# Performance work log

Measured on AMD Instinct MI355X. Metric: run time of the kernel, lower is better.

Reference implementation:

```python
import jax, jax.numpy as jnp
import numpy as np

N_EMBD = 512
NUM_HEADS = 8
HEAD_SIZE = 64


def setup_inputs() -> dict:
    key = jax.random.key(0)
    ks = jax.random.split(key, 6)
    B, T, C, H, D = 64, 256, N_EMBD, NUM_HEADS, HEAD_SIZE
    s = 0.02
    return {
        "x": jax.random.normal(ks[0], (B, T, C), dtype=jnp.float32),
        "wq": jax.random.normal(ks[1], (H, C, D), dtype=jnp.float32) * s,
        "wk": jax.random.normal(ks[2], (H, C, D), dtype=jnp.float32) * s,
        "wv": jax.random.normal(ks[3], (H, C, D), dtype=jnp.float32) * s,
        "bq": jnp.zeros((H, D), dtype=jnp.float32),
        "bk": jnp.zeros((H, D), dtype=jnp.float32),
        "bv": jnp.zeros((H, D), dtype=jnp.float32),
        "wo": jax.random.normal(ks[4], (H * D, C), dtype=jnp.float32) * s,
        "bo": jnp.zeros((C,), dtype=jnp.float32),
    }


def reference(x, wq, wk, wv, bq, bk, bv, wo, bo):
    B, T, C = x.shape
    H, _, D = wq.shape
    # per-head QKV projections (vectorized over heads)
    q = jnp.einsum('btc,hcd->bhtd', x, wq) + bq[None, :, None, :]
    k = jnp.einsum('btc,hcd->bhtd', x, wk) + bk[None, :, None, :]
    v = jnp.einsum('btc,hcd->bhtd', x, wv) + bv[None, :, None, :]
    scale = 1.0 / jnp.sqrt(jnp.asarray(D, dtype=x.dtype))
    scores = jnp.einsum('bhtd,bhsd->bhts', q, k) * scale  # [B,H,T,T]
    causal = jnp.tril(jnp.ones((T, T), dtype=bool))
    scores = jnp.where(causal[None, None], scores, -jnp.inf)
    weights = jax.nn.softmax(scores, axis=-1)  # dropout omitted (eval mode)
    out = jnp.einsum('bhts,bhsd->bhtd', weights, v)  # [B,H,T,D]
    combined = out.transpose(0, 2, 1, 3).reshape(B, T, H * D)
    return combined @ wo + bo
```

## Files before the change

### kernel.cpp

```cpp
#include <hip/hip_runtime.h>

typedef unsigned int   u32;
typedef unsigned short u16;
typedef __attribute__((ext_vector_type(8))) short short8;
typedef __attribute__((ext_vector_type(4))) float f32x4;


__device__ __forceinline__ u16 f2bf(float f) {
    u32 u = __float_as_uint(f);
    u += 0x7fffu + ((u >> 16) & 1u);
    return (u16)(u >> 16);
}

__device__ __forceinline__ void gload_lds16(const u16* g, u16* l) {
    __builtin_amdgcn_global_load_lds(
        (const __attribute__((address_space(1))) u32*)(const void*)g,
        (__attribute__((address_space(3))) u32*)(void*)l, 16, 0, 0);
}

__global__ void cast_x_kernel(const float* __restrict__ x, u16* __restrict__ xb) {
    int i = blockIdx.x * 256 + threadIdx.x;
    float4 v = ((const float4*)x)[i];
    ushort4 o;
    o.x = f2bf(v.x); o.y = f2bf(v.y); o.z = f2bf(v.z); o.w = f2bf(v.w);
    ((ushort4*)xb)[i] = o;
}

__global__ void pack_wqkv_kernel(const float* __restrict__ wq, const float* __restrict__ wk,
                                 const float* __restrict__ wv, u16* __restrict__ wt) {
    int i = blockIdx.x * 256 + threadIdx.x;
    int n = i >> 9, c = i & 511;
    int proj = n >> 9, hd = n & 511;
    int h = hd >> 6, d = hd & 63;
    const float* w = (proj == 0) ? wq : (proj == 1) ? wk : wv;
    wt[(size_t)n * 512 + c] = f2bf(w[h * 32768 + c * 64 + d]);
}

__global__ void pack_wo_kernel(const float* __restrict__ wo, u16* __restrict__ wt) {
    int i = blockIdx.x * 256 + threadIdx.x;
    int n = i >> 9, k = i & 511;
    wt[(size_t)n * 512 + k] = f2bf(wo[(size_t)k * 512 + n]);
}

template<int EPI, int NT>
__global__ __launch_bounds__(256)
void gemm128_kernel(const u16* __restrict__ A, const u16* __restrict__ Bt,
                    float* __restrict__ outf, const float* __restrict__ bo,
                    u16* __restrict__ Qb, u16* __restrict__ Kb, u16* __restrict__ Vb,
                    const float* __restrict__ bq, const float* __restrict__ bk,
                    const float* __restrict__ bv) {
    __shared__ __align__(16) u16 As[3][128 * 32];
    __shared__ __align__(16) u16 Bs[3][128 * 32];
    const int tid = threadIdx.x;
    const int bid = blockIdx.x;
    const int xcd = bid & 7;
    const int k8  = bid >> 3;
    const int m0 = (xcd * 16 + k8 / NT) * 128;
    const int n0 = (k8 % NT) * 128;
    const int lrow = tid >> 2;
    const int seg  = tid & 3;
    const int xsw  = (lrow >> 1) & 3;
    const u16* Ag = A  + (size_t)(m0 + lrow) * 512 + (seg ^ xsw) * 8;
    const u16* Bg = Bt + (size_t)(n0 + lrow) * 512 + (seg ^ xsw) * 8;
    const int lofs = lrow * 32 + seg * 8;

    const int w = tid >> 6, lane = tid & 63;
    const int wrow = (w >> 1) * 64, wcol = (w & 1) * 64;
    const int lm = lane & 15, quad = lane >> 4;
    const int kx = (quad ^ ((lm >> 1) & 3)) * 8;

    f32x4 acc[4][4] = {};

    gload_lds16(Ag,            As[0] + lofs);
    gload_lds16(Ag + 64 * 512, As[0] + lofs + 64 * 32);
    gload_lds16(Bg,            Bs[0] + lofs);
    gload_lds16(Bg + 64 * 512, Bs[0] + lofs + 64 * 32);

    #pragma unroll 1
    for (int kt = 0; kt < 16; ++kt) {
        __syncthreads();
        if (kt < 15) {
            const u16* Agp = Ag + (kt + 1) * 32;
            const u16* Bgp = Bg + (kt + 1) * 32;
            u16* Asp = As[(kt + 1) % 3] + lofs;
            u16* Bsp = Bs[(kt + 1) % 3] + lofs;
            gload_lds16(Agp,            Asp);
            gload_lds16(Agp + 64 * 512, Asp + 64 * 32);
            gload_lds16(Bgp,            Bsp);
            gload_lds16(Bgp + 64 * 512, Bsp + 64 * 32);
        }
        const u16* Ac = As[kt % 3];
        const u16* Bc = Bs[kt % 3];
        short8 af[4], bf[4];
        #pragma unroll
        for (int mi = 0; mi < 4; ++mi)
            af[mi] = *(const short8*)(Ac + (wrow + mi * 16 + lm) * 32 + kx);
        #pragma unroll
        for (int ni = 0; ni < 4; ++ni)
            bf[ni] = *(const short8*)(Bc + (wcol + ni * 16 + lm) * 32 + kx);
        #pragma unroll
        for (int mi = 0; mi < 4; ++mi)
            #pragma unroll
            for (int ni = 0; ni < 4; ++ni)
                acc[mi][ni] = __builtin_amdgcn_mfma_f32_16x16x32_bf16(af[mi], bf[ni], acc[mi][ni], 0, 0, 0);
    }

    if (EPI == 1) {
        #pragma unroll
        for (int ni = 0; ni < 4; ++ni) {
            int ncol = n0 + wcol + ni * 16 + lm;
            float bias = bo[ncol];
            #pragma unroll
            for (int mi = 0; mi < 4; ++mi) {
                int mbase = m0 + wrow + mi * 16 + quad * 4;
                #pragma unroll
                for (int r = 0; r < 4; ++r)
                    outf[(size_t)(mbase + r) * 512 + ncol] = acc[mi][ni][r] + bias;
            }
        }
    } else {
        #pragma unroll
        for (int ni = 0; ni < 4; ++ni) {
            int ncol = n0 + wcol + ni * 16 + lm;
            int proj = ncol >> 9, hd = ncol & 511;
            int h = hd >> 6, d = hd & 63;
            const float* bptr = (proj == 0) ? bq : (proj == 1) ? bk : bv;
            u16* dst = (proj == 0) ? Qb : (proj == 1) ? Kb : Vb;
            float bias = bptr[hd];
            #pragma unroll
            for (int mi = 0; mi < 4; ++mi) {
                int mbase = m0 + wrow + mi * 16 + quad * 4;
                #pragma unroll
                for (int r = 0; r < 4; ++r) {
                    int mrow = mbase + r;
                    int b = mrow >> 8, t = mrow & 255;
                    size_t idx = (proj == 2)
                        ? ((size_t)((b * 8 + h) * 64 + d) * 256 + t)
                        : ((size_t)((b * 8 + h) * 256 + t) * 64 + d);
                    dst[idx] = f2bf(acc[mi][ni][r] + bias);
                }
            }
        }
    }
}

__global__ __launch_bounds__(256)
void attn_mfma_kernel(const u16* __restrict__ Qg, const u16* __restrict__ Kg,
                      const u16* __restrict__ Vtg, u16* __restrict__ attn) {
    __shared__ __align__(16) u16 lds[20480];
    const int bid = blockIdx.x;
    const int head = (bid & 7) * 64 + ((bid >> 3) >> 1);
    const int iset = (bid >> 3) & 1;
    const int b = head >> 3, h = head & 7;
    const int tid = threadIdx.x;
    const size_t hb = (size_t)head * 16384;

    {
        const uint4* Ksrc = (const uint4*)(Kg + hb);
        uint4* L4 = (uint4*)lds;
        #pragma unroll
        for (int it = 0; it < 8; ++it) {
            int g = it * 256 + tid;
            int kr = g >> 3, kc = g & 7;
            L4[kr * 8 + (kc ^ (kr & 7))] = Ksrc[g];
        }
    }
    __syncthreads();

    const int w = tid >> 6, lane = tid & 63;
    const int lm = lane & 15, quad = lane >> 4;
    const int l7 = lm & 7;

    const int kx0 = (quad ^ l7) * 8;
    const int kx1 = ((4 + quad) ^ l7) * 8;
    const u16* Kbase = lds + lm * 64;
    const u16* Vg = Vtg + hb;
    const int Pbase = 16384 + w * 1024;
    const int x0 = (lm >> 3) & 1;
    const int pw_even = Pbase + quad * 16 + l7 + x0 * 8;
    const int pw_odd  = Pbase + quad * 16 + l7 + (x0 ^ 1) * 8;
    const int pr0 = Pbase + ((lm & 3) * 4 + (quad >> 1)) * 64
                  + (2 * (lm >> 2) + ((quad & 1) ^ (lm & 1))) * 8;

    #pragma unroll 1
    for (int ii = 0; ii < 2; ++ii) {
        const int i = iset ? (ii ? 2 : 1) : (ii ? 3 : 0);
        const int t0 = i * 64 + w * 16;
        short8 qa0 = *(const short8*)(Qg + hb + (size_t)(t0 + lm) * 64 + quad * 8);
        short8 qa1 = *(const short8*)(Qg + hb + (size_t)(t0 + lm) * 64 + 32 + quad * 8);
        f32x4 O[4] = {};
        float mr[4] = {-INFINITY, -INFINITY, -INFINITY, -INFINITY};
        float lr[4] = {0.f, 0.f, 0.f, 0.f};

        #pragma unroll 1
        for (int j = 0; j <= i; ++j) {
            f32x4 S[4] = {};
            #pragma unroll
            for (int ni = 0; ni < 4; ++ni) {
                const u16* kp = Kbase + j * 4096 + ni * 1024;
                short8 kb0 = *(const short8*)(kp + kx0);
                short8 kb1 = *(const short8*)(kp + kx1);
                S[ni] = __builtin_amdgcn_mfma_f32_16x16x32_bf16(qa0, kb0, S[ni], 0, 0, 0);
                S[ni] = __builtin_amdgcn_mfma_f32_16x16x32_bf16(qa1, kb1, S[ni], 0, 0, 0);
            }
            short8 vb[4][2];
            #pragma unroll
            for (int nd = 0; nd < 4; ++nd) {
                const u16* vp = Vg + (size_t)(nd * 16 + lm) * 256 + j * 64;
                vb[nd][0] = *(const short8*)(vp + quad * 8);
                vb[nd][1] = *(const short8*)(vp + 32 + quad * 8);
            }
            if (j == i) {
                #pragma unroll
                for (int ni = 0; ni < 4; ++ni) {
                    int scol = ni * 16 + lm;
                    #pragma unroll
                    for (int rr = 0; rr < 4; ++rr) {
                        int tloc = w * 16 + quad * 4 + rr;
                        S[ni][rr] = (scol > tloc) ? -INFINITY : S[ni][rr] * 0.125f;
                    }
                }
            } else {
                #pragma unroll
                for (int ni = 0; ni < 4; ++ni)
                    #pragma unroll
                    for (int rr = 0; rr < 4; ++rr)
                        S[ni][rr] *= 0.125f;
            }
            float alpha[4];
            #pragma unroll
            for (int rr = 0; rr < 4; ++rr) {
                float mx = fmaxf(fmaxf(S[0][rr], S[1][rr]), fmaxf(S[2][rr], S[3][rr]));
                mx = fmaxf(mx, __shfl_xor(mx, 1));
                mx = fmaxf(mx, __shfl_xor(mx, 2));
                mx = fmaxf(mx, __shfl_xor(mx, 4));
                mx = fmaxf(mx, __shfl_xor(mx, 8));
                float mnew = fmaxf(mr[rr], mx);
                alpha[rr] = __expf(mr[rr] - mnew);
                mr[rr] = mnew;
            }
            float rs[4] = {0.f, 0.f, 0.f, 0.f};
            #pragma unroll
            for (int ni = 0; ni < 4; ++ni) {
                #pragma unroll
                for (int rr = 0; rr < 4; ++rr) {
                    float p = __expf(S[ni][rr] - mr[rr]);
                    rs[rr] += p;
                    int addr = ((rr & 1) ? pw_odd : pw_even) + (rr * 4 + ni) * 64;
                    lds[addr] = f2bf(p);
                }
            }
            #pragma unroll
            for (int rr = 0; rr < 4; ++rr) {
                float s = rs[rr];
                s += __shfl_xor(s, 1);
                s += __shfl_xor(s, 2);
                s += __shfl_xor(s, 4);
                s += __shfl_xor(s, 8);
                lr[rr] = lr[rr] * alpha[rr] + s;
                O[0][rr] *= alpha[rr]; O[1][rr] *= alpha[rr];
                O[2][rr] *= alpha[rr]; O[3][rr] *= alpha[rr];
            }
            __syncthreads();
            short8 pa0 = *(const short8*)(lds + pr0);
            short8 pa1 = *(const short8*)(lds + pr0 + 128);
            #pragma unroll
            for (int nd = 0; nd < 4; ++nd) {
                O[nd] = __builtin_amdgcn_mfma_f32_16x16x32_bf16(pa0, vb[nd][0], O[nd], 0, 0, 0);
                O[nd] = __builtin_amdgcn_mfma_f32_16x16x32_bf16(pa1, vb[nd][1], O[nd], 0, 0, 0);
            }
        }
        #pragma unroll
        for (int rr = 0; rr < 4; ++rr) {
            float inv = 1.0f / lr[rr];
            int t = t0 + quad * 4 + rr;
            u16* op = attn + (size_t)(b * 256 + t) * 512 + h * 64 + lm;
            op[0]  = f2bf(O[0][rr] * inv);
            op[16] = f2bf(O[1][rr] * inv);
            op[32] = f2bf(O[2][rr] * inv);
            op[48] = f2bf(O[3][rr] * inv);
        }
    }
}

extern "C" void kernel_launch(void* const* d_in, const int* in_sizes, int n_in,
                              void* d_out, int out_size, void* d_ws, size_t ws_size,
                              hipStream_t stream) {
    const float* x  = (const float*)d_in[0];
    const float* wq = (const float*)d_in[1];
    const float* wk = (const float*)d_in[2];
    const float* wv = (const float*)d_in[3];
    const float* bq = (const float*)d_in[4];
    const float* bk = (const float*)d_in[5];
    const float* bv = (const float*)d_in[6];
    const float* wo = (const float*)d_in[7];
    const float* bo = (const float*)d_in[8];
    float* out = (float*)d_out;

    char* ws = (char*)d_ws;
    const size_t SZ = 16777216;
    u16* xb    = (u16*)(ws);
    u16* Qb    = (u16*)(ws + SZ);
    u16* Kb    = (u16*)(ws + 2 * SZ);
    u16* Vt    = (u16*)(ws + 3 * SZ);
    u16* attn  = (u16*)(ws + 4 * SZ);
    u16* wqkvT = (u16*)(ws + 5 * SZ);
    u16* woT   = (u16*)(ws + 5 * SZ + 1572864);

    cast_x_kernel<<<8192, 256, 0, stream>>>(x, xb);
    pack_wqkv_kernel<<<3072, 256, 0, stream>>>(wq, wk, wv, wqkvT);
    pack_wo_kernel<<<1024, 256, 0, stream>>>(wo, woT);

    gemm128_kernel<0, 12><<<1536, 256, 0, stream>>>(
        xb, wqkvT, nullptr, nullptr, Qb, Kb, Vt, bq, bk, bv);

    attn_mfma_kernel<<<1024, 256, 0, stream>>>(Qb, Kb, Vt, attn);

    gemm128_kernel<1, 4><<<512, 256, 0, stream>>>(
        attn, woT, out, bo, nullptr, nullptr, nullptr, nullptr, nullptr, nullptr);
}
```

Before: 215.6 us.

## Replace direct-to-LDS loads with register-staged prefetch pipeline in GEMMs

Both GEMM kernels stop using global_load_lds with a triple LDS buffer. Instead they prefetch three k-tiles ahead into registers, write the next tile into a double LDS buffer while the MFMAs run, and synchronise with a custom barrier that waits only on lgkmcnt. The goal is to hide global memory latency more deeply and overlap LDS stores with compute. The cost is more VGPRs for the staging registers. The custom barrier does not wait on vmcnt, so it depends on the compiler inserting that wait before each register-to-LDS store.

Result: slower. 332.3 us (+54.1%).

```diff
diff --git a/kernel.cpp b/kernel.cpp
--- a/kernel.cpp
+++ b/kernel.cpp
@@ -12,10 +12,8 @@
     return (u16)(u >> 16);
 }
 
-__device__ __forceinline__ void gload_lds16(const u16* g, u16* l) {
-    __builtin_amdgcn_global_load_lds(
-        (const __attribute__((address_space(1))) u32*)(const void*)g,
-        (__attribute__((address_space(3))) u32*)(void*)l, 16, 0, 0);
+__device__ __forceinline__ void wg_barrier() {
+    __asm__ volatile("s_waitcnt lgkmcnt(0)\n\ts_barrier" ::: "memory");
 }
 
 __global__ void cast_x_kernel(const float* __restrict__ x, u16* __restrict__ xb) {
@@ -44,13 +42,13 @@
 
 template<int EPI, int NT>
 __global__ __launch_bounds__(256)
-void gemm128_kernel(const u16* __restrict__ A, const u16* __restrict__ Bt,
-                    float* __restrict__ outf, const float* __restrict__ bo,
-                    u16* __restrict__ Qb, u16* __restrict__ Kb, u16* __restrict__ Vb,
-                    const float* __restrict__ bq, const float* __restrict__ bk,
-                    const float* __restrict__ bv) {
-    __shared__ __align__(16) u16 As[3][128 * 32];
-    __shared__ __align__(16) u16 Bs[3][128 * 32];
+void gemm_pipe(const u16* __restrict__ A, const u16* __restrict__ Bt,
+               float* __restrict__ outf, const float* __restrict__ bo,
+               u16* __restrict__ Qb, u16* __restrict__ Kb, u16* __restrict__ Vb,
+               const float* __restrict__ bq, const float* __restrict__ bk,
+               const float* __restrict__ bv) {
+    __shared__ __align__(16) u16 As[2][4096];
+    __shared__ __align__(16) u16 Bs[2][4096];
     const int tid = threadIdx.x;
     const int bid = blockIdx.x;
     const int xcd = bid & 7;
@@ -69,28 +67,31 @@
     const int lm = lane & 15, quad = lane >> 4;
     const int kx = (quad ^ ((lm >> 1) & 3)) * 8;
 
+    uint4 ra0[3], ra1[3], rb0[3], rb1[3];
+
+    #define LDSET(s, kt) do {                                        \
+        ra0[s] = *(const uint4*)(Ag + (kt) * 32);                    \
+        ra1[s] = *(const uint4*)(Ag + 64 * 512 + (kt) * 32);         \
+        rb0[s] = *(const uint4*)(Bg + (kt) * 32);                    \
+        rb1[s] = *(const uint4*)(Bg + 64 * 512 + (kt) * 32);         \
+    } while (0)
+    #define STSET(buf, s) do {                                       \
+        *(uint4*)(As[buf] + lofs)           = ra0[s];                \
+        *(uint4*)(As[buf] + lofs + 64 * 32) = ra1[s];                \
+        *(uint4*)(Bs[buf] + lofs)           = rb0[s];                \
+        *(uint4*)(Bs[buf] + lofs + 64 * 32) = rb1[s];                \
+    } while (0)
+
     f32x4 acc[4][4] = {};
 
-    gload_lds16(Ag,            As[0] + lofs);
-    gload_lds16(Ag + 64 * 512, As[0] + lofs + 64 * 32);
-    gload_lds16(Bg,            Bs[0] + lofs);
-    gload_lds16(Bg + 64 * 512, Bs[0] + lofs + 64 * 32);
+    LDSET(0, 0); LDSET(1, 1); LDSET(2, 2);
+    STSET(0, 0);
+    wg_barrier();
 
     #pragma unroll 1
     for (int kt = 0; kt < 16; ++kt) {
-        __syncthreads();
-        if (kt < 15) {
-            const u16* Agp = Ag + (kt + 1) * 32;
-            const u16* Bgp = Bg + (kt + 1) * 32;
-            u16* Asp = As[(kt + 1) % 3] + lofs;
-            u16* Bsp = Bs[(kt + 1) % 3] + lofs;
-            gload_lds16(Agp,            Asp);
-            gload_lds16(Agp + 64 * 512, Asp + 64 * 32);
-            gload_lds16(Bgp,            Bsp);
-            gload_lds16(Bgp + 64 * 512, Bsp + 64 * 32);
-        }
-        const u16* Ac = As[kt % 3];
-        const u16* Bc = Bs[kt % 3];
+        const u16* Ac = As[kt & 1];
+        const u16* Bc = Bs[kt & 1];
         short8 af[4], bf[4];
         #pragma unroll
         for (int mi = 0; mi < 4; ++mi)
@@ -98,12 +99,17 @@
         #pragma unroll
         for (int ni = 0; ni < 4; ++ni)
             bf[ni] = *(const short8*)(Bc + (wcol + ni * 16 + lm) * 32 + kx);
+        if (kt < 15) STSET((kt + 1) & 1, (kt + 1) % 3);
+        if (kt < 13) LDSET(kt % 3, kt + 3);
         #pragma unroll
         for (int mi = 0; mi < 4; ++mi)
             #pragma unroll
             for (int ni = 0; ni < 4; ++ni)
                 acc[mi][ni] = __builtin_amdgcn_mfma_f32_16x16x32_bf16(af[mi], bf[ni], acc[mi][ni], 0, 0, 0);
+        wg_barrier();
     }
+    #undef LDSET
+    #undef STSET
 
     if (EPI == 1) {
         #pragma unroll
@@ -311,11 +317,11 @@
     pack_wqkv_kernel<<<3072, 256, 0, stream>>>(wq, wk, wv, wqkvT);
     pack_wo_kernel<<<1024, 256, 0, stream>>>(wo, woT);
 
-    gemm128_kernel<0, 12><<<1536, 256, 0, stream>>>(
+    gemm_pipe<0, 12><<<1536, 256, 0, stream>>>(
         xb, wqkvT, nullptr, nullptr, Qb, Kb, Vt, bq, bk, bv);
 
     attn_mfma_kernel<<<1024, 256, 0, stream>>>(Qb, Kb, Vt, attn);
 
-    gemm128_kernel<1, 4><<<512, 256, 0, stream>>>(
+    gemm_pipe<1, 4><<<512, 256, 0, stream>>>(
         attn, woT, out, bo, nullptr, nullptr, nullptr, nullptr, nullptr, nullptr);
 }
```
